# Kernel tuning notes

Hardware: AMD Instinct MI355X
Metric: run time of the kernel (lower is better)

Reference implementation:

```python
import jax, jax.numpy as jnp
import numpy as np
import math

B, H, W, C = 4, 64, 64, 512
G = 32  # GroupNorm groups
EPS = 1e-6


def setup_inputs() -> dict:
    key = jax.random.key(0)
    ks = jax.random.split(key, 6)
    wscale = 1.0 / math.sqrt(C)
    return {
        "x": jax.random.normal(ks[0], (B, H, W, C), jnp.float32),
        "gn_scale": jnp.ones((C,), jnp.float32),
        "gn_bias": jnp.zeros((C,), jnp.float32),
        "wq": jax.random.normal(ks[1], (C, C), jnp.float32) * wscale,
        "bq": jnp.zeros((C,), jnp.float32),
        "wk": jax.random.normal(ks[2], (C, C), jnp.float32) * wscale,
        "bk": jnp.zeros((C,), jnp.float32),
        "wv": jax.random.normal(ks[3], (C, C), jnp.float32) * wscale,
        "bv": jnp.zeros((C,), jnp.float32),
        "wo": jax.random.normal(ks[4], (C, C), jnp.float32) * wscale,
        "bo": jnp.zeros((C,), jnp.float32),
    }


def _group_norm(x, scale, bias):
    # flax nnx.GroupNorm: stats over (H, W, channels-within-group)
    b, h, w, c = x.shape
    xg = x.reshape(b, h, w, G, c // G)
    mean = jnp.mean(xg, axis=(1, 2, 4), keepdims=True)
    var = jnp.mean(jnp.square(xg - mean), axis=(1, 2, 4), keepdims=True)
    xg = (xg - mean) * jax.lax.rsqrt(var + EPS)
    return xg.reshape(b, h, w, c) * scale + bias


def reference(x, gn_scale, gn_bias, wq, bq, wk, bk, wv, bv, wo, bo):
    b, h, w, c = x.shape
    n = h * w
    h_ = _group_norm(x, gn_scale, gn_bias)
    hf = h_.reshape(b, n, c)  # 1x1 conv == per-token matmul
    q = hf @ wq + bq
    k = hf @ wk + bk
    v = hf @ wv + bv
    scale = 1.0 / math.sqrt(c)
    attn = jax.nn.softmax(jnp.einsum('bqc,bkc->bqk', q, k) * scale, axis=-1)
    o = jnp.einsum('bqk,bkc->bqc', attn, v)
    o = o @ wo + bo
    return x + o.reshape(b, h, w, c)
```

## Files before the change

kernel.cpp:

```cpp
#include <hip/hip_runtime.h>
#include <hip/hip_bf16.h>
#include <math.h>


typedef __bf16 bf16;
typedef float f32x4 __attribute__((ext_vector_type(4)));
typedef __bf16 bf16x8 __attribute__((ext_vector_type(8)));
typedef __bf16 bf16x4 __attribute__((ext_vector_type(4)));
typedef long long i64;

#define AS1 __attribute__((address_space(1)))
#define AS3 __attribute__((address_space(3)))

#define NB   4
#define NTOK 4096
#define CCH  512
#define NGRP 32

__device__ __forceinline__ void gload_lds16(const void* g, void* l) {
  __builtin_amdgcn_global_load_lds((AS1 void*)(g), (AS3 void*)(l), 16, 0, 0);
}

__device__ __forceinline__ unsigned char to_e4m3(float f) {
#if __has_builtin(__builtin_amdgcn_cvt_pk_fp8_f32)
  return (unsigned char)(__builtin_amdgcn_cvt_pk_fp8_f32(f, 0.f, 0, false) & 0xff);
#else
  const unsigned u = __float_as_uint(f);
  const unsigned s = (u >> 24) & 0x80;
  const float a = fabsf(f);
  if (a >= 448.f) return (unsigned char)(s | 0x7E);
  if (a < 0.015625f) {
    const int m = (int)rintf(a * 512.f);
    return (unsigned char)(s | m);
  }
  int e = (int)((u >> 23) & 0xff) - 127;
  const float q = exp2f((float)(e - 3));
  int r = (int)rintf(a / q);
  if (r == 16) { e += 1; r = 8; }
  return (unsigned char)(s | ((e + 7) << 3) | (r - 8));
#endif
}

__global__ __launch_bounds__(256) void gn_partial(const float4* __restrict__ x4,
                                                  float* __restrict__ partials) {
  const int chunk = blockIdx.x, b = blockIdx.y;
  const int tid = threadIdx.x;
  const size_t base = ((size_t)b * NTOK + (size_t)chunk * 64) * 128;
  float s = 0.f, ss = 0.f;
  #pragma unroll 4
  for (int it = 0; it < 32; ++it) {
    const float4 v = x4[base + it * 256 + tid];
    s  += v.x + v.y + v.z + v.w;
    ss += v.x * v.x + v.y * v.y + v.z * v.z + v.w * v.w;
  }
  __shared__ float ls[256], lss[256];
  ls[tid] = s; lss[tid] = ss;
  __syncthreads();
  if (tid < 32) {
    float ps = 0.f, pss = 0.f;
    #pragma unroll
    for (int j = 0; j < 4; ++j) {
      ps  += ls[tid * 4 + j] + ls[128 + tid * 4 + j];
      pss += lss[tid * 4 + j] + lss[128 + tid * 4 + j];
    }
    const size_t o = (((size_t)b * 64 + chunk) * 32 + tid) * 2;
    partials[o] = ps; partials[o + 1] = pss;
  }
}

__global__ __launch_bounds__(128) void gn_reduce(const float* __restrict__ partials,
                                                 float* __restrict__ stats) {
  const int tid = threadIdx.x;
  const int b = tid >> 5, g = tid & 31;
  float s = 0.f, ss = 0.f;
  for (int c = 0; c < 64; ++c) {
    const size_t o = (((size_t)b * 64 + c) * 32 + g) * 2;
    s += partials[o]; ss += partials[o + 1];
  }
  const float inv = 1.f / (NTOK * 16.f);
  const float mean = s * inv;
  const float var = ss * inv - mean * mean;
  stats[tid * 2] = mean;
  stats[tid * 2 + 1] = rsqrtf(var + 1e-6f);
}

__global__ __launch_bounds__(256) void gn_apply(const float4* __restrict__ x4,
                                                const float* __restrict__ stats,
                                                const float* __restrict__ gsc,
                                                const float* __restrict__ gbi,
                                                bf16* __restrict__ hf) {
  const int i = blockIdx.x * 256 + threadIdx.x;
  const float4 v = x4[i];
  const size_t e = (size_t)i * 4;
  const int c = (int)(e & (CCH - 1));
  const int b = (int)(e >> 21);
  const int g = c >> 4;
  const float mean = stats[(b * NGRP + g) * 2];
  const float rstd = stats[(b * NGRP + g) * 2 + 1];
  bf16x4 o;
  o[0] = (bf16)((v.x - mean) * rstd * gsc[c + 0] + gbi[c + 0]);
  o[1] = (bf16)((v.y - mean) * rstd * gsc[c + 1] + gbi[c + 1]);
  o[2] = (bf16)((v.z - mean) * rstd * gsc[c + 2] + gbi[c + 2]);
  o[3] = (bf16)((v.w - mean) * rstd * gsc[c + 3] + gbi[c + 3]);
  *reinterpret_cast<bf16x4*>(&hf[e]) = o;
}

__global__ __launch_bounds__(256) void wcast_t(const float* __restrict__ wq,
                                               const float* __restrict__ wk,
                                               const float* __restrict__ bq,
                                               const float* __restrict__ bk,
                                               bf16* __restrict__ dst,
                                               float* __restrict__ bcat) {
  const int w = blockIdx.y;
  const float* src = (w == 0) ? wq : wk;
  bf16* out = dst + (size_t)w * CCH * CCH;
  const int t = blockIdx.x;
  const int tr = t >> 3, tc = t & 7;
  if (t == 0) {
    const float* bsrc = (w == 0) ? bq : bk;
    for (int i = threadIdx.x; i < CCH; i += 256) bcat[w * CCH + i] = bsrc[i];
  }
  __shared__ float tile[64][65];
  for (int i = threadIdx.x; i < 4096; i += 256) {
    const int r = i >> 6, c = i & 63;
    tile[r][c] = src[(size_t)(tr * 64 + r) * CCH + tc * 64 + c];
  }
  __syncthreads();
  for (int i = threadIdx.x; i < 4096; i += 256) {
    const int r = i >> 6, c = i & 63;
    out[(size_t)(tc * 64 + r) * CCH + tr * 64 + c] = (bf16)tile[c][r];
  }
}

__global__ __launch_bounds__(256) void prep_w(const float* __restrict__ wv,
                                              const float* __restrict__ wo,
                                              const float* __restrict__ bv,
                                              const float* __restrict__ bo,
                                              bf16* __restrict__ wpT,
                                              float* __restrict__ bpv) {
  const int ta = blockIdx.x >> 3, tb = blockIdx.x & 7;
  __shared__ float woS[64][65];
  __shared__ float wvS[64][65];
  const int t = threadIdx.x;
  if (blockIdx.x == 0) {
    for (int j = t; j < CCH; j += 256) {
      float a2 = bo[j];
      for (int k2 = 0; k2 < CCH; ++k2) a2 += bv[k2] * wo[(size_t)k2 * CCH + j];
      bpv[j] = a2;
    }
  }
  const int aa0 = (t & 15) * 4, bb0 = (t >> 4) * 4;
  float acc[4][4] = {};
  for (int kt = 0; kt < CCH; kt += 64) {
    for (int i = t; i < 4096; i += 256) {
      const int r = i >> 6, c = i & 63;
      woS[r][c] = wo[(size_t)(kt + r) * CCH + ta * 64 + c];
      wvS[r][c] = wv[(size_t)(tb * 64 + r) * CCH + kt + c];
    }
    __syncthreads();
    #pragma unroll 8
    for (int kk = 0; kk < 64; ++kk) {
      float wo4[4], wv4[4];
      #pragma unroll
      for (int i2 = 0; i2 < 4; ++i2) { wo4[i2] = woS[kk][aa0 + i2]; wv4[i2] = wvS[bb0 + i2][kk]; }
      #pragma unroll
      for (int a2 = 0; a2 < 4; ++a2)
        #pragma unroll
        for (int b2 = 0; b2 < 4; ++b2)
          acc[a2][b2] += wo4[a2] * wv4[b2];
    }
    __syncthreads();
  }
  #pragma unroll
  for (int a2 = 0; a2 < 4; ++a2)
    #pragma unroll
    for (int b2 = 0; b2 < 4; ++b2)
      wpT[(size_t)(ta * 64 + aa0 + a2) * CCH + tb * 64 + bb0 + b2] = (bf16)acc[a2][b2];
}

__global__ __launch_bounds__(256) void rowsum_inv(const float* __restrict__ partials,
                                                  float* __restrict__ rinv) {
  const int row = blockIdx.x * 256 + threadIdx.x;
  const float* p = partials + (size_t)row * 32;
  float s = 0.f;
  #pragma unroll
  for (int j = 0; j < 32; ++j) s += p[j];
  rinv[row] = 1.f / s;
}

template <int EPI>
__global__ __launch_bounds__(512, 2) void gemm256(
    const bf16* __restrict__ A, int lda,
    const bf16* __restrict__ Bt, int ldb,
    unsigned char* __restrict__ C, int ldc,
    const float* __restrict__ bias,
    int M, int N, int K) {
  constexpr int BK = 64;
  constexpr int BNt = 128;
  constexpr int WN = 32;
  constexpr int NREP = 2;

  __shared__ bf16 Al[2][256 * BK];
  __shared__ bf16 Bl[2][BNt * BK];

  const int tid = threadIdx.x;
  const int lane = tid & 63;
  const int wave = tid >> 6;
  const int wm = wave >> 2, wn = wave & 3;
  const int fr = lane & 15, fq = lane >> 4;
  const int nbn = N / BNt;
  int bm, bn;
  if constexpr (EPI == 4) {
    const int nwg = gridDim.x;
    const int bx = (blockIdx.x & 7) * (nwg >> 3) + (blockIdx.x >> 3);
    bm = bx / nbn; bn = bx % nbn;
  } else {
    const int r = blockIdx.x & 7, q = blockIdx.x >> 3;
    const int pg = q / nbn;
    bm = r + 8 * pg;
    bn = q - pg * nbn;
  }

  const int srow = tid >> 3;
  const int scol = (((tid & 7) ^ (srow & 7)) * 8);
  const bf16* Ab = A + (size_t)(bm * 256 + srow) * lda + scol;
  const bf16* Bb = Bt + (size_t)(bn * BNt + srow) * ldb + scol;

  const int xk = fr & 7;
  const int c0 = ((0 + fq) ^ xk) * 8;
  const int c1 = ((4 + fq) ^ xk) * 8;
  const int aroff = (wm * 128 + fr) * BK;
  const int broff = (wn * WN + fr) * BK;

  f32x4 acc[8][NREP];
  #pragma unroll
  for (int m2 = 0; m2 < 8; ++m2)
    #pragma unroll
    for (int n2 = 0; n2 < NREP; ++n2)
      acc[m2][n2] = f32x4{0.f, 0.f, 0.f, 0.f};
  bf16x8 af[4][2];
  bf16x8 bfr[NREP][2];

#define STAGE_A(buf, h, kt)                                                     \
  { gload_lds16(Ab + (size_t)((h) * 128) * lda + (kt),                          \
                &Al[buf][(h) * 8192 + wave * 512]);                             \
    gload_lds16(Ab + (size_t)((h) * 128 + 64) * lda + (kt),                     \
                &Al[buf][(h) * 8192 + 4096 + wave * 512]); }
#define STAGE_B(buf, h, kt)                                                     \
  gload_lds16(Bb + (size_t)((h) * 64) * ldb + (kt),                             \
              &Bl[buf][(h) * 4096 + wave * 512]);
#define LOADA(buf, mh)                                                          \
  { _Pragma("unroll") for (int mi = 0; mi < 4; ++mi) {                          \
      af[mi][0] = *(const bf16x8*)&Al[buf][aroff + ((mh) * 64 + mi * 16) * BK + c0]; \
      af[mi][1] = *(const bf16x8*)&Al[buf][aroff + ((mh) * 64 + mi * 16) * BK + c1]; } }
#define LOADB(buf)                                                              \
  { _Pragma("unroll") for (int ni = 0; ni < NREP; ++ni) {                       \
      bfr[ni][0] = *(const bf16x8*)&Bl[buf][broff + (ni * 16) * BK + c0];       \
      bfr[ni][1] = *(const bf16x8*)&Bl[buf][broff + (ni * 16) * BK + c1]; } }
#define MMA(mh)                                                                 \
  { __builtin_amdgcn_s_setprio(1);                                              \
    _Pragma("unroll") for (int ks = 0; ks < 2; ++ks)                            \
      _Pragma("unroll") for (int mi = 0; mi < 4; ++mi)                          \
        _Pragma("unroll") for (int ni = 0; ni < NREP; ++ni)                     \
          acc[(mh) * 4 + mi][ni] = __builtin_amdgcn_mfma_f32_16x16x32_bf16(     \
              af[mi][ks], bfr[ni][ks], acc[(mh) * 4 + mi][ni], 0, 0, 0);        \
    __builtin_amdgcn_s_setprio(0); }
#define BARX() __builtin_amdgcn_s_barrier()
#define PIN() __builtin_amdgcn_sched_barrier(0)
#define LGKM0() { asm volatile("s_waitcnt lgkmcnt(0)" ::: "memory"); PIN(); }
#define VMW(n) asm volatile("s_waitcnt vmcnt(" #n ")" ::: "memory")

  STAGE_A(0, 0, 0); STAGE_A(0, 1, 0);
  STAGE_B(0, 0, 0); STAGE_B(0, 1, 0);
  STAGE_A(1, 0, BK); STAGE_B(1, 0, BK);
  VMW(3);
  BARX();

  const int niter = K >> 7;
  for (int j = 0; j < niter; ++j) {
    const int kt1 = j * 128 + 64;
    const int kt2 = kt1 + 64, kt3 = kt1 + 128;
    const bool last = (j == niter - 1);
    LOADA(0, 0); LOADB(0); STAGE_A(1, 1, kt1); STAGE_B(1, 1, kt1);
    PIN(); BARX(); LGKM0(); MMA(0); BARX();
    LOADA(0, 1); if (!last) { STAGE_A(0, 0, kt2); STAGE_B(0, 0, kt2); }
    PIN(); BARX(); LGKM0(); MMA(1);
    if (last) { VMW(0); } else VMW(3);
    BARX();
    LOADA(1, 0); LOADB(1); if (!last) { STAGE_A(0, 1, kt2); STAGE_B(0, 1, kt2); }
    PIN(); BARX(); LGKM0(); MMA(0); BARX();
    LOADA(1, 1); if (!last) { STAGE_A(1, 0, kt3); STAGE_B(1, 0, kt3); }
    PIN(); BARX(); LGKM0(); MMA(1);
    if (!last) VMW(3);
    BARX();
  }

  const int crow0 = bm * 256 + wm * 128 + fq * 4;
  const int ccol0 = bn * BNt + wn * WN + fr;
  #pragma unroll
  for (int mh = 0; mh < 2; ++mh)
    #pragma unroll
    for (int mi = 0; mi < 4; ++mi)
      #pragma unroll
      for (int nr = 0; nr < NREP; ++nr)
        #pragma unroll
        for (int jj = 0; jj < 4; ++jj) {
          const int row = crow0 + mh * 64 + mi * 16 + jj;
          const int col = ccol0 + nr * 16;
          const float val = acc[mh * 4 + mi][nr][jj];
          const size_t idx = (size_t)row * ldc + col;
          if constexpr (EPI == 0) {
            C[idx] = to_e4m3(val + bias[col]);
          } else {
            C[idx] = to_e4m3(val);
          }
        }
#undef STAGE_A
#undef STAGE_B
#undef LOADA
#undef LOADB
#undef MMA
#undef BARX
#undef PIN
#undef LGKM0
#undef VMW
}

__global__ __launch_bounds__(512, 4) void scores_fp8(
    const unsigned char* __restrict__ qk,
    unsigned char* __restrict__ S8,
    float* __restrict__ partials,
    float sscale) {
  __shared__ unsigned char Ql[2][16384];
  __shared__ unsigned char Kl[2][8192];
  const int bb = blockIdx.y;
  const unsigned char* Aq = qk + (size_t)bb * NTOK * 1024;
  const int tid = threadIdx.x, lane = tid & 63, wave = tid >> 6;
  const int wm = wave >> 2, wn = wave & 3;
  const int fr = lane & 15, fq = lane >> 4;
  const int r_ = blockIdx.x & 7, q_ = blockIdx.x >> 3;
  const int pg = q_ >> 5;
  const int bm = r_ + 8 * pg, bn = q_ & 31;

  const int sr = tid >> 2;
  const int aswz = ((tid & 3) ^ ((tid >> 3) & 3)) * 16;
  const unsigned char* Ab = Aq + (size_t)(bm * 256 + sr) * 1024 + aswz;
  const unsigned char* Bb = Aq + (size_t)(bn * 128 + sr) * 1024 + 512 + aswz;

  const int xA = fr & 6;
  const int c0 = (fq ^ xA) * 8;
  const int c1 = ((fq ^ 4) ^ xA) * 8;

  f32x4 acc[8][2];
  #pragma unroll
  for (int m2 = 0; m2 < 8; ++m2)
    #pragma unroll
    for (int n2 = 0; n2 < 2; ++n2)
      acc[m2][n2] = f32x4{0.f, 0.f, 0.f, 0.f};
  i64 af8[4][2], bf8[2][2];

#define SSTAGE_A(buf, kt)                                                       \
  { gload_lds16(Ab + (kt), (char*)&Ql[buf][0] + tid * 16);                      \
    gload_lds16(Ab + (size_t)128 * 1024 + (kt), (char*)&Ql[buf][0] + 8192 + tid * 16); }
#define SSTAGE_B(buf, kt)                                                       \
  gload_lds16(Bb + (kt), (char*)&Kl[buf][0] + tid * 16);
#define SLOADA(buf, mh)                                                         \
  { _Pragma("unroll") for (int mi = 0; mi < 4; ++mi) {                          \
      const int ro = (wm * 128 + (mh) * 64 + mi * 16 + fr) * 64;                \
      af8[mi][0] = *(const i64*)&Ql[buf][ro + c0];                              \
      af8[mi][1] = *(const i64*)&Ql[buf][ro + c1]; } }
#define SLOADB(buf)                                                             \
  { _Pragma("unroll") for (int ni = 0; ni < 2; ++ni) {                          \
      const int ro = (wn * 32 + ni * 16 + fr) * 64;                             \
      bf8[ni][0] = *(const i64*)&Kl[buf][ro + c0];                              \
      bf8[ni][1] = *(const i64*)&Kl[buf][ro + c1]; } }
#define SMMA(mh)                                                                \
  { __builtin_amdgcn_s_setprio(1);                                              \
    _Pragma("unroll") for (int ks = 0; ks < 2; ++ks)                            \
      _Pragma("unroll") for (int mi = 0; mi < 4; ++mi)                          \
        _Pragma("unroll") for (int ni = 0; ni < 2; ++ni)                        \
          acc[(mh) * 4 + mi][ni] = __builtin_amdgcn_mfma_f32_16x16x32_fp8_fp8(  \
              af8[mi][ks], bf8[ni][ks], acc[(mh) * 4 + mi][ni], 0, 0, 0);       \
    __builtin_amdgcn_s_setprio(0); }
#define SBARX() __builtin_amdgcn_s_barrier()
#define SPIN() __builtin_amdgcn_sched_barrier(0)
#define SLGKM0() { asm volatile("s_waitcnt lgkmcnt(0)" ::: "memory"); SPIN(); }
#define SVMW(n) asm volatile("s_waitcnt vmcnt(" #n ")" ::: "memory")

  SSTAGE_B(0, 0); SSTAGE_A(0, 0); SSTAGE_B(1, 64);
  SVMW(1);
  SBARX();

  const int niter = 4;
  for (int j = 0; j < niter; ++j) {
    const int kt0 = j * 128;
    const bool last = (j == niter - 1);
    SLOADA(0, 0); SLOADB(0); SSTAGE_A(1, kt0 + 64);
    SPIN(); SBARX(); SLGKM0(); SMMA(0); SBARX();
    SLOADA(0, 1); if (!last) SSTAGE_B(0, kt0 + 128);
    SPIN(); SBARX(); SLGKM0(); SMMA(1);
    if (last) { SVMW(0); } else { SVMW(1); }
    SBARX();
    SLOADA(1, 0); SLOADB(1); if (!last) SSTAGE_A(0, kt0 + 128);
    SPIN(); SBARX(); SLGKM0(); SMMA(0); SBARX();
    SLOADA(1, 1); if (!last) SSTAGE_B(1, kt0 + 192);
    SPIN(); SBARX(); SLGKM0(); SMMA(1);
    if (last) { SVMW(0); } else { SVMW(1); }
    SBARX();
  }

  unsigned char* Cb = S8 + (size_t)bb * NTOK * NTOK;
  const int crow0 = bm * 256 + wm * 128 + fq * 4;
  const int ccol0 = bn * 128 + wn * 32 + fr;
  float* sums = (float*)&Ql[0][0];
  #pragma unroll
  for (int mh = 0; mh < 2; ++mh)
    #pragma unroll
    for (int mi = 0; mi < 4; ++mi)
      #pragma unroll
      for (int jj = 0; jj < 4; ++jj) {
        const int row = crow0 + mh * 64 + mi * 16 + jj;
        float rs = 0.f;
        #pragma unroll
        for (int ni = 0; ni < 2; ++ni) {
          const float e = __expf(fminf(acc[mh * 4 + mi][ni][jj] * sscale, 6.10f));
          rs += e;
          Cb[(size_t)row * NTOK + ccol0 + ni * 16] = to_e4m3(e);
        }
        rs += __shfl_xor(rs, 1); rs += __shfl_xor(rs, 2);
        rs += __shfl_xor(rs, 4); rs += __shfl_xor(rs, 8);
        if (fr == 0)
          sums[(wm * 128 + mh * 64 + mi * 16 + fq * 4 + jj) * 4 + wn] = rs;
      }
  __syncthreads();
  if (tid < 256) {
    const float s4 = sums[tid * 4] + sums[tid * 4 + 1] +
                     sums[tid * 4 + 2] + sums[tid * 4 + 3];
    partials[((size_t)bb * NTOK + bm * 256 + tid) * 32 + bn] = s4;
  }
#undef SSTAGE_A
#undef SSTAGE_B
#undef SLOADA
#undef SLOADB
#undef SMMA
#undef SBARX
#undef SPIN
#undef SLGKM0
#undef SVMW
}

__global__ __launch_bounds__(512, 2) void pv_fp8(
    const unsigned char* __restrict__ S8,
    const unsigned char* __restrict__ V8,
    float* __restrict__ out, const float* __restrict__ bpv,
    const float* __restrict__ x, const float* __restrict__ rinv, int vofs) {
  __shared__ unsigned char Sl[2][16384];
  __shared__ unsigned char Vl[2][8192];
  const int bb = blockIdx.y;
  const unsigned char* A8 = S8 + (size_t)bb * NTOK * NTOK;
  const int tid = threadIdx.x, lane = tid & 63, wave = tid >> 6;
  const int wm = wave >> 2, wn = wave & 3;
  const int fr = lane & 15, fq = lane >> 4;
  const int r_ = blockIdx.x & 7, q_ = blockIdx.x >> 3;
  const int pg = q_ >> 2;
  const int bm = r_ + 8 * pg, bn = q_ & 3;

  const int sr = tid >> 2;
  const int aswz = ((tid & 3) ^ ((tid >> 3) & 3)) * 16;
  const unsigned char* Ab = A8 + (size_t)(bm * 256 + sr) * NTOK + aswz;
  const unsigned char* Bb = V8 + (size_t)(bn * 128 + sr) * (NB * NTOK)
                            + vofs + bb * NTOK + aswz;

  const int xA = fr & 6;
  const int c0 = (fq ^ xA) * 8;
  const int c1 = ((fq ^ 4) ^ xA) * 8;

  f32x4 acc[8][2];
  #pragma unroll
  for (int m2 = 0; m2 < 8; ++m2)
    #pragma unroll
    for (int n2 = 0; n2 < 2; ++n2)
      acc[m2][n2] = f32x4{0.f, 0.f, 0.f, 0.f};
  i64 af8[4][2], bf8[2][2];

#define PSTAGE_A(buf, kt)                                                       \
  { gload_lds16(Ab + (kt), (char*)&Sl[buf][0] + tid * 16);                      \
    gload_lds16(Ab + (size_t)128 * NTOK + (kt), (char*)&Sl[buf][0] + 8192 + tid * 16); }
#define PSTAGE_B(buf, kt)                                                       \
  gload_lds16(Bb + (kt), (char*)&Vl[buf][0] + tid * 16);
#define PLOADA(buf, mh)                                                         \
  { _Pragma("unroll") for (int mi = 0; mi < 4; ++mi) {                          \
      const int ro = (wm * 128 + (mh) * 64 + mi * 16 + fr) * 64;                \
      af8[mi][0] = *(const i64*)&Sl[buf][ro + c0];                              \
      af8[mi][1] = *(const i64*)&Sl[buf][ro + c1]; } }
#define PLOADB(buf)                                                             \
  { _Pragma("unroll") for (int ni = 0; ni < 2; ++ni) {                          \
      const int ro = (wn * 32 + ni * 16 + fr) * 64;                             \
      bf8[ni][0] = *(const i64*)&Vl[buf][ro + c0];                              \
      bf8[ni][1] = *(const i64*)&Vl[buf][ro + c1]; } }
#define PMMA(mh)                                                                \
  { __builtin_amdgcn_s_setprio(1);                                              \
    _Pragma("unroll") for (int ks = 0; ks < 2; ++ks)                            \
      _Pragma("unroll") for (int mi = 0; mi < 4; ++mi)                          \
        _Pragma("unroll") for (int ni = 0; ni < 2; ++ni)                        \
          acc[(mh) * 4 + mi][ni] = __builtin_amdgcn_mfma_f32_16x16x32_fp8_fp8(  \
              af8[mi][ks], bf8[ni][ks], acc[(mh) * 4 + mi][ni], 0, 0, 0);       \
    __builtin_amdgcn_s_setprio(0); }
#define PBARX() __builtin_amdgcn_s_barrier()
#define PPIN() __builtin_amdgcn_sched_barrier(0)
#define PLGKM0() { asm volatile("s_waitcnt lgkmcnt(0)" ::: "memory"); PPIN(); }
#define PVMW(n) asm volatile("s_waitcnt vmcnt(" #n ")" ::: "memory")

  PSTAGE_B(0, 0); PSTAGE_A(0, 0); PSTAGE_B(1, 64);
  PVMW(1);
  PBARX();

  const int niter = 32;
  for (int j = 0; j < niter; ++j) {
    const int kt0 = j * 128;
    const bool last = (j == niter - 1);
    PLOADA(0, 0); PLOADB(0); PSTAGE_A(1, kt0 + 64);
    PPIN(); PBARX(); PLGKM0(); PMMA(0); PBARX();
    PLOADA(0, 1); if (!last) PSTAGE_B(0, kt0 + 128);
    PPIN(); PBARX(); PLGKM0(); PMMA(1);
    if (last) { PVMW(0); } else { PVMW(1); }
    PBARX();
    PLOADA(1, 0); PLOADB(1); if (!last) PSTAGE_A(0, kt0 + 128);
    PPIN(); PBARX(); PLGKM0(); PMMA(0); PBARX();
    PLOADA(1, 1); if (!last) PSTAGE_B(1, kt0 + 192);
    PPIN(); PBARX(); PLGKM0(); PMMA(1);
    if (last) { PVMW(0); } else { PVMW(1); }
    PBARX();
  }

  const int crow0 = bm * 256 + wm * 128 + fq * 4;
  const int ccol0 = bn * 128 + wn * 32 + fr;
  #pragma unroll
  for (int mh = 0; mh < 2; ++mh)
    #pragma unroll
    for (int mi = 0; mi < 4; ++mi)
      #pragma unroll
      for (int jj = 0; jj < 4; ++jj) {
        const int row = crow0 + mh * 64 + mi * 16 + jj;
        const float ri = rinv[(size_t)bb * NTOK + row];
        #pragma unroll
        for (int ni = 0; ni < 2; ++ni) {
          const int col = ccol0 + ni * 16;
          const size_t idx = ((size_t)bb * NTOK + row) * CCH + col;
          out[idx] = acc[mh * 4 + mi][ni][jj] * ri + bpv[col] + x[idx];
        }
      }
#undef PSTAGE_A
#undef PSTAGE_B
#undef PLOADA
#undef PLOADB
#undef PMMA
#undef PBARX
#undef PPIN
#undef PLGKM0
#undef PVMW
}

extern "C" void kernel_launch(void* const* d_in, const int* in_sizes, int n_in,
                              void* d_out, int out_size, void* d_ws, size_t ws_size,
                              hipStream_t stream) {
  const float* x   = (const float*)d_in[0];
  const float* gsc = (const float*)d_in[1];
  const float* gbi = (const float*)d_in[2];
  const float* wq  = (const float*)d_in[3];
  const float* bq  = (const float*)d_in[4];
  const float* wk  = (const float*)d_in[5];
  const float* bk  = (const float*)d_in[6];
  const float* wv  = (const float*)d_in[7];
  const float* bv  = (const float*)d_in[8];
  const float* wo  = (const float*)d_in[9];
  const float* bo  = (const float*)d_in[10];
  float* out = (float*)d_out;
  char* ws = (char*)d_ws;

  const float sscale = 0.044194173824159216f;
  const bool batched = ws_size >= 96082944ULL;

  if (batched) {
    unsigned char* S8  = (unsigned char*)(ws + 0);
    bf16*  hf    = (bf16*)(ws + 0);
    unsigned char* qk8 = (unsigned char*)(ws + 67108864);
    unsigned char* vt8 = (unsigned char*)(ws + 83886080);
    bf16*  wT    = (bf16*)(ws + 92274688);
    float* bcat  = (float*)(ws + 93847552);
    float* bpv   = (float*)(ws + 93851648);
    float* stats = (float*)(ws + 93853696);
    float* parts = (float*)(ws + 93854720);
    float* spart = (float*)(ws + 93920256);
    float* rinv  = (float*)(ws + 96017408);

    gn_partial<<<dim3(64, NB), 256, 0, stream>>>((const float4*)x, parts);
    gn_reduce<<<1, 128, 0, stream>>>(parts, stats);
    gn_apply<<<8192, 256, 0, stream>>>((const float4*)x, stats, gsc, gbi, hf);
    wcast_t<<<dim3(64, 2), 256, 0, stream>>>(wq, wk, bq, bk, wT, bcat);
    prep_w<<<64, 256, 0, stream>>>(wv, wo, bv, bo, wT + 2 * CCH * CCH, bpv);

    gemm256<0><<<dim3(512, 1), 512, 0, stream>>>(
        hf, 512, wT, 512, qk8, 1024, bcat, 16384, 1024, 512);
    gemm256<4><<<dim3(256, 1), 512, 0, stream>>>(
        wT + 2 * CCH * CCH, 512, hf, 512, vt8, 16384, nullptr, 512, 16384, 512);
    scores_fp8<<<dim3(512, NB), 512, 0, stream>>>(qk8, S8, spart, sscale);
    rowsum_inv<<<64, 256, 0, stream>>>(spart, rinv);
    pv_fp8<<<dim3(64, NB), 512, 0, stream>>>(S8, vt8, out, bpv, x, rinv, 0);
  } else {
    unsigned char* S81 = (unsigned char*)(ws + 0);
    bf16*  hf    = (bf16*)(ws + 0);
    unsigned char* qk8 = (unsigned char*)(ws + 16777216);
    unsigned char* vt8 = (unsigned char*)(ws + 33554432);
    bf16*  wT    = (bf16*)(ws + 41943040);
    float* bcat  = (float*)(ws + 43515904);
    float* bpv   = (float*)(ws + 43520000);
    float* stats = (float*)(ws + 43522048);
    float* parts = (float*)(ws + 43523072);
    float* spart = (float*)(ws + 43588608);
    float* rinv  = (float*)(ws + 44112896);

    gn_partial<<<dim3(64, NB), 256, 0, stream>>>((const float4*)x, parts);
    gn_reduce<<<1, 128, 0, stream>>>(parts, stats);
    gn_apply<<<8192, 256, 0, stream>>>((const float4*)x, stats, gsc, gbi, hf);
    wcast_t<<<dim3(64, 2), 256, 0, stream>>>(wq, wk, bq, bk, wT, bcat);
    prep_w<<<64, 256, 0, stream>>>(wv, wo, bv, bo, wT + 2 * CCH * CCH, bpv);
    gemm256<0><<<dim3(512, 1), 512, 0, stream>>>(
        hf, 512, wT, 512, qk8, 1024, bcat, 16384, 1024, 512);
    gemm256<4><<<dim3(256, 1), 512, 0, stream>>>(
        wT + 2 * CCH * CCH, 512, hf, 512, vt8, 16384, nullptr, 512, 16384, 512);
    for (int b = 0; b < NB; ++b) {
      scores_fp8<<<dim3(512, 1), 512, 0, stream>>>(
          qk8 + (size_t)b * NTOK * 1024, S81, spart, sscale);
      rowsum_inv<<<16, 256, 0, stream>>>(spart, rinv);
      pv_fp8<<<dim3(64, 1), 512, 0, stream>>>(
          S81, vt8, out + (size_t)b * NTOK * CCH, bpv,
          x + (size_t)b * NTOK * CCH, rinv, b * NTOK);
    }
  }
}
```

Measured before the change: 288.8 us.

## Permute fp8 K-layout for 16-byte LDS reads and single-buffer 128-wide K tiles

The projection GEMM and the scores kernel now write fp8 outputs with a column permutation inside each 128-wide group. Along with a new 8-way XOR swizzle, this lets the scores and PV kernels fetch both k-steps' MFMA operands with one 16-byte LDS read instead of two 8-byte reads. The double-buffered, barrier-pinned pipeline with 64-wide K stages is replaced by a simple single-buffered loop over 128-wide K tiles that waits for all loads before computing. pv_fp8 occupancy hint rises from 2 to 4 blocks. This cuts LDS instruction count and complexity, but gives up overlap of global loads with MFMA work, which may hurt the long PV loop.

Result: faster. 270.6 us (-6.3%).

```diff
diff --git a/kernel.cpp b/kernel.cpp
--- a/kernel.cpp
+++ b/kernel.cpp
@@ -8,6 +8,7 @@
 typedef __bf16 bf16x8 __attribute__((ext_vector_type(8)));
 typedef __bf16 bf16x4 __attribute__((ext_vector_type(4)));
 typedef long long i64;
+typedef __attribute__((ext_vector_type(2))) long long i64x2;
 
 #define AS1 __attribute__((address_space(1)))
 #define AS3 __attribute__((address_space(3)))
@@ -39,6 +40,12 @@
   if (r == 16) { e += 1; r = 8; }
   return (unsigned char)(s | ((e + 7) << 3) | (r - 8));
 #endif
+}
+
+__device__ __forceinline__ int kperm(int col) {
+  const int g = (col >> 3) & 15;
+  const int gp = (g & 3) * 4 + (g >> 2);
+  return (col & ~127) | (gp * 8) | (col & 7);
 }
 
 __global__ __launch_bounds__(256) void gn_partial(const float4* __restrict__ x4,
@@ -308,7 +315,7 @@
           const int row = crow0 + mh * 64 + mi * 16 + jj;
           const int col = ccol0 + nr * 16;
           const float val = acc[mh * 4 + mi][nr][jj];
-          const size_t idx = (size_t)row * ldc + col;
+          const size_t idx = (size_t)row * ldc + kperm(col);
           if constexpr (EPI == 0) {
             C[idx] = to_e4m3(val + bias[col]);
           } else {
@@ -331,8 +338,8 @@
     unsigned char* __restrict__ S8,
     float* __restrict__ partials,
     float sscale) {
-  __shared__ unsigned char Ql[2][16384];
-  __shared__ unsigned char Kl[2][8192];
+  __shared__ unsigned char Ql[256 * 128];
+  __shared__ unsigned char Kl[128 * 128];
   const int bb = blockIdx.y;
   const unsigned char* Aq = qk + (size_t)bb * NTOK * 1024;
   const int tid = threadIdx.x, lane = tid & 63, wave = tid >> 6;
@@ -342,14 +349,14 @@
   const int pg = q_ >> 5;
   const int bm = r_ + 8 * pg, bn = q_ & 31;
 
-  const int sr = tid >> 2;
-  const int aswz = ((tid & 3) ^ ((tid >> 3) & 3)) * 16;
-  const unsigned char* Ab = Aq + (size_t)(bm * 256 + sr) * 1024 + aswz;
-  const unsigned char* Bb = Aq + (size_t)(bn * 128 + sr) * 1024 + 512 + aswz;
-
-  const int xA = fr & 6;
-  const int c0 = (fq ^ xA) * 8;
-  const int c1 = ((fq ^ 4) ^ xA) * 8;
+  const int sr = tid >> 3;
+  const int ssl = ((tid & 7) ^ (sr & 7)) * 16;
+  const unsigned char* Ab = Aq + (size_t)(bm * 256 + sr) * 1024 + ssl;
+  const unsigned char* Bb = Aq + (size_t)(bn * 128 + sr) * 1024 + 512 + ssl;
+
+  const int xk = fr & 7;
+  const int sA0 = ((2 * fq + 0) ^ xk) * 16;
+  const int sA1 = ((2 * fq + 1) ^ xk) * 16;
 
   f32x4 acc[8][2];
   #pragma unroll
@@ -357,62 +364,49 @@
     #pragma unroll
     for (int n2 = 0; n2 < 2; ++n2)
       acc[m2][n2] = f32x4{0.f, 0.f, 0.f, 0.f};
-  i64 af8[4][2], bf8[2][2];
-
-#define SSTAGE_A(buf, kt)                                                       \
-  { gload_lds16(Ab + (kt), (char*)&Ql[buf][0] + tid * 16);                      \
-    gload_lds16(Ab + (size_t)128 * 1024 + (kt), (char*)&Ql[buf][0] + 8192 + tid * 16); }
-#define SSTAGE_B(buf, kt)                                                       \
-  gload_lds16(Bb + (kt), (char*)&Kl[buf][0] + tid * 16);
-#define SLOADA(buf, mh)                                                         \
-  { _Pragma("unroll") for (int mi = 0; mi < 4; ++mi) {                          \
-      const int ro = (wm * 128 + (mh) * 64 + mi * 16 + fr) * 64;                \
-      af8[mi][0] = *(const i64*)&Ql[buf][ro + c0];                              \
-      af8[mi][1] = *(const i64*)&Ql[buf][ro + c1]; } }
-#define SLOADB(buf)                                                             \
-  { _Pragma("unroll") for (int ni = 0; ni < 2; ++ni) {                          \
-      const int ro = (wn * 32 + ni * 16 + fr) * 64;                             \
-      bf8[ni][0] = *(const i64*)&Kl[buf][ro + c0];                              \
-      bf8[ni][1] = *(const i64*)&Kl[buf][ro + c1]; } }
-#define SMMA(mh)                                                                \
-  { __builtin_amdgcn_s_setprio(1);                                              \
-    _Pragma("unroll") for (int ks = 0; ks < 2; ++ks)                            \
-      _Pragma("unroll") for (int mi = 0; mi < 4; ++mi)                          \
-        _Pragma("unroll") for (int ni = 0; ni < 2; ++ni)                        \
-          acc[(mh) * 4 + mi][ni] = __builtin_amdgcn_mfma_f32_16x16x32_fp8_fp8(  \
-              af8[mi][ks], bf8[ni][ks], acc[(mh) * 4 + mi][ni], 0, 0, 0);       \
-    __builtin_amdgcn_s_setprio(0); }
-#define SBARX() __builtin_amdgcn_s_barrier()
-#define SPIN() __builtin_amdgcn_sched_barrier(0)
-#define SLGKM0() { asm volatile("s_waitcnt lgkmcnt(0)" ::: "memory"); SPIN(); }
-#define SVMW(n) asm volatile("s_waitcnt vmcnt(" #n ")" ::: "memory")
-
-  SSTAGE_B(0, 0); SSTAGE_A(0, 0); SSTAGE_B(1, 64);
-  SVMW(1);
-  SBARX();
-
-  const int niter = 4;
-  for (int j = 0; j < niter; ++j) {
-    const int kt0 = j * 128;
-    const bool last = (j == niter - 1);
-    SLOADA(0, 0); SLOADB(0); SSTAGE_A(1, kt0 + 64);
-    SPIN(); SBARX(); SLGKM0(); SMMA(0); SBARX();
-    SLOADA(0, 1); if (!last) SSTAGE_B(0, kt0 + 128);
-    SPIN(); SBARX(); SLGKM0(); SMMA(1);
-    if (last) { SVMW(0); } else { SVMW(1); }
-    SBARX();
-    SLOADA(1, 0); SLOADB(1); if (!last) SSTAGE_A(0, kt0 + 128);
-    SPIN(); SBARX(); SLGKM0(); SMMA(0); SBARX();
-    SLOADA(1, 1); if (!last) SSTAGE_B(1, kt0 + 192);
-    SPIN(); SBARX(); SLGKM0(); SMMA(1);
-    if (last) { SVMW(0); } else { SVMW(1); }
-    SBARX();
+
+  for (int it = 0; it < 4; ++it) {
+    const int kt = it * 128;
+    #pragma unroll
+    for (int i = 0; i < 4; ++i)
+      gload_lds16(Ab + (size_t)(i * 64) * 1024 + kt, (char*)Ql + i * 8192 + tid * 16);
+    #pragma unroll
+    for (int i = 0; i < 2; ++i)
+      gload_lds16(Bb + (size_t)(i * 64) * 1024 + kt, (char*)Kl + i * 8192 + tid * 16);
+    asm volatile("s_waitcnt vmcnt(0)" ::: "memory");
+    __syncthreads();
+    #pragma unroll
+    for (int t = 0; t < 2; ++t) {
+      const int sl = (t == 0) ? sA0 : sA1;
+      i64x2 bfv[2];
+      #pragma unroll
+      for (int ni = 0; ni < 2; ++ni)
+        bfv[ni] = *(const i64x2*)&Kl[(wn * 32 + ni * 16 + fr) * 128 + sl];
+      #pragma unroll
+      for (int mh = 0; mh < 2; ++mh) {
+        i64x2 afv[4];
+        #pragma unroll
+        for (int mi = 0; mi < 4; ++mi)
+          afv[mi] = *(const i64x2*)&Ql[(wm * 128 + mh * 64 + mi * 16 + fr) * 128 + sl];
+        __builtin_amdgcn_s_setprio(1);
+        #pragma unroll
+        for (int ks = 0; ks < 2; ++ks)
+          #pragma unroll
+          for (int mi = 0; mi < 4; ++mi)
+            #pragma unroll
+            for (int ni = 0; ni < 2; ++ni)
+              acc[mh * 4 + mi][ni] = __builtin_amdgcn_mfma_f32_16x16x32_fp8_fp8(
+                  afv[mi][ks], bfv[ni][ks], acc[mh * 4 + mi][ni], 0, 0, 0);
+        __builtin_amdgcn_s_setprio(0);
+      }
+    }
+    __syncthreads();
   }
 
   unsigned char* Cb = S8 + (size_t)bb * NTOK * NTOK;
   const int crow0 = bm * 256 + wm * 128 + fq * 4;
   const int ccol0 = bn * 128 + wn * 32 + fr;
-  float* sums = (float*)&Ql[0][0];
+  float* sums = (float*)&Ql[0];
   #pragma unroll
   for (int mh = 0; mh < 2; ++mh)
     #pragma unroll
@@ -425,7 +419,7 @@
         for (int ni = 0; ni < 2; ++ni) {
           const float e = __expf(fminf(acc[mh * 4 + mi][ni][jj] * sscale, 6.10f));
           rs += e;
-          Cb[(size_t)row * NTOK + ccol0 + ni * 16] = to_e4m3(e);
+          Cb[(size_t)row * NTOK + kperm(ccol0 + ni * 16)] = to_e4m3(e);
         }
         rs += __shfl_xor(rs, 1); rs += __shfl_xor(rs, 2);
         rs += __shfl_xor(rs, 4); rs += __shfl_xor(rs, 8);
@@ -438,24 +432,15 @@
                      sums[tid * 4 + 2] + sums[tid * 4 + 3];
     partials[((size_t)bb * NTOK + bm * 256 + tid) * 32 + bn] = s4;
   }
-#undef SSTAGE_A
-#undef SSTAGE_B
-#undef SLOADA
-#undef SLOADB
-#undef SMMA
-#undef SBARX
-#undef SPIN
-#undef SLGKM0
-#undef SVMW
-}
-
-__global__ __launch_bounds__(512, 2) void pv_fp8(
+}
+
+__global__ __launch_bounds__(512, 4) void pv_fp8(
     const unsigned char* __restrict__ S8,
     const unsigned char* __restrict__ V8,
     float* __restrict__ out, const float* __restrict__ bpv,
     const float* __restrict__ x, const float* __restrict__ rinv, int vofs) {
-  __shared__ unsigned char Sl[2][16384];
-  __shared__ unsigned char Vl[2][8192];
+  __shared__ unsigned char Sl[256 * 128];
+  __shared__ unsigned char Vl[128 * 128];
   const int bb = blockIdx.y;
   const unsigned char* A8 = S8 + (size_t)bb * NTOK * NTOK;
   const int tid = threadIdx.x, lane = tid & 63, wave = tid >> 6;
@@ -465,15 +450,15 @@
   const int pg = q_ >> 2;
   const int bm = r_ + 8 * pg, bn = q_ & 3;
 
-  const int sr = tid >> 2;
-  const int aswz = ((tid & 3) ^ ((tid >> 3) & 3)) * 16;
-  const unsigned char* Ab = A8 + (size_t)(bm * 256 + sr) * NTOK + aswz;
+  const int sr = tid >> 3;
+  const int ssl = ((tid & 7) ^ (sr & 7)) * 16;
+  const unsigned char* Ab = A8 + (size_t)(bm * 256 + sr) * NTOK + ssl;
   const unsigned char* Bb = V8 + (size_t)(bn * 128 + sr) * (NB * NTOK)
-                            + vofs + bb * NTOK + aswz;
-
-  const int xA = fr & 6;
-  const int c0 = (fq ^ xA) * 8;
-  const int c1 = ((fq ^ 4) ^ xA) * 8;
+                            + vofs + bb * NTOK + ssl;
+
+  const int xk = fr & 7;
+  const int sA0 = ((2 * fq + 0) ^ xk) * 16;
+  const int sA1 = ((2 * fq + 1) ^ xk) * 16;
 
   f32x4 acc[8][2];
   #pragma unroll
@@ -481,56 +466,43 @@
     #pragma unroll
     for (int n2 = 0; n2 < 2; ++n2)
       acc[m2][n2] = f32x4{0.f, 0.f, 0.f, 0.f};
-  i64 af8[4][2], bf8[2][2];
-
-#define PSTAGE_A(buf, kt)                                                       \
-  { gload_lds16(Ab + (kt), (char*)&Sl[buf][0] + tid * 16);                      \
-    gload_lds16(Ab + (size_t)128 * NTOK + (kt), (char*)&Sl[buf][0] + 8192 + tid * 16); }
-#define PSTAGE_B(buf, kt)                                                       \
-  gload_lds16(Bb + (kt), (char*)&Vl[buf][0] + tid * 16);
-#define PLOADA(buf, mh)                                                         \
-  { _Pragma("unroll") for (int mi = 0; mi < 4; ++mi) {                          \
-      const int ro = (wm * 128 + (mh) * 64 + mi * 16 + fr) * 64;                \
-      af8[mi][0] = *(const i64*)&Sl[buf][ro + c0];                              \
-      af8[mi][1] = *(const i64*)&Sl[buf][ro + c1]; } }
-#define PLOADB(buf)                                                             \
-  { _Pragma("unroll") for (int ni = 0; ni < 2; ++ni) {                          \
-      const int ro = (wn * 32 + ni * 16 + fr) * 64;                             \
-      bf8[ni][0] = *(const i64*)&Vl[buf][ro + c0];                              \
-      bf8[ni][1] = *(const i64*)&Vl[buf][ro + c1]; } }
-#define PMMA(mh)                                                                \
-  { __builtin_amdgcn_s_setprio(1);                                              \
-    _Pragma("unroll") for (int ks = 0; ks < 2; ++ks)                            \
-      _Pragma("unroll") for (int mi = 0; mi < 4; ++mi)                          \
-        _Pragma("unroll") for (int ni = 0; ni < 2; ++ni)                        \
-          acc[(mh) * 4 + mi][ni] = __builtin_amdgcn_mfma_f32_16x16x32_fp8_fp8(  \
-              af8[mi][ks], bf8[ni][ks], acc[(mh) * 4 + mi][ni], 0, 0, 0);       \
-    __builtin_amdgcn_s_setprio(0); }
-#define PBARX() __builtin_amdgcn_s_barrier()
-#define PPIN() __builtin_amdgcn_sched_barrier(0)
-#define PLGKM0() { asm volatile("s_waitcnt lgkmcnt(0)" ::: "memory"); PPIN(); }
-#define PVMW(n) asm volatile("s_waitcnt vmcnt(" #n ")" ::: "memory")
-
-  PSTAGE_B(0, 0); PSTAGE_A(0, 0); PSTAGE_B(1, 64);
-  PVMW(1);
-  PBARX();
-
-  const int niter = 32;
-  for (int j = 0; j < niter; ++j) {
-    const int kt0 = j * 128;
-    const bool last = (j == niter - 1);
-    PLOADA(0, 0); PLOADB(0); PSTAGE_A(1, kt0 + 64);
-    PPIN(); PBARX(); PLGKM0(); PMMA(0); PBARX();
-    PLOADA(0, 1); if (!last) PSTAGE_B(0, kt0 + 128);
-    PPIN(); PBARX(); PLGKM0(); PMMA(1);
-    if (last) { PVMW(0); } else { PVMW(1); }
-    PBARX();
-    PLOADA(1, 0); PLOADB(1); if (!last) PSTAGE_A(0, kt0 + 128);
-    PPIN(); PBARX(); PLGKM0(); PMMA(0); PBARX();
-    PLOADA(1, 1); if (!last) PSTAGE_B(1, kt0 + 192);
-    PPIN(); PBARX(); PLGKM0(); PMMA(1);
-    if (last) { PVMW(0); } else { PVMW(1); }
-    PBARX();
+
+  for (int it = 0; it < 32; ++it) {
+    const int kt = it * 128;
+    #pragma unroll
+    for (int i = 0; i < 4; ++i)
+      gload_lds16(Ab + (size_t)(i * 64) * NTOK + kt, (char*)Sl + i * 8192 + tid * 16);
+    #pragma unroll
+    for (int i = 0; i < 2; ++i)
+      gload_lds16(Bb + (size_t)(i * 64) * (NB * NTOK) + kt, (char*)Vl + i * 8192 + tid * 16);
+    asm volatile("s_waitcnt vmcnt(0)" ::: "memory");
+    __syncthreads();
+    #pragma unroll
+    for (int t = 0; t < 2; ++t) {
+      const int sl = (t == 0) ? sA0 : sA1;
+      i64x2 bfv[2];
+      #pragma unroll
+      for (int ni = 0; ni < 2; ++ni)
+        bfv[ni] = *(const i64x2*)&Vl[(wn * 32 + ni * 16 + fr) * 128 + sl];
+      #pragma unroll
+      for (int mh = 0; mh < 2; ++mh) {
+        i64x2 afv[4];
+        #pragma unroll
+        for (int mi = 0; mi < 4; ++mi)
+          afv[mi] = *(const i64x2*)&Sl[(wm * 128 + mh * 64 + mi * 16 + fr) * 128 + sl];
+        __builtin_amdgcn_s_setprio(1);
+        #pragma unroll
+        for (int ks = 0; ks < 2; ++ks)
+          #pragma unroll
+          for (int mi = 0; mi < 4; ++mi)
+            #pragma unroll
+            for (int ni = 0; ni < 2; ++ni)
+              acc[mh * 4 + mi][ni] = __builtin_amdgcn_mfma_f32_16x16x32_fp8_fp8(
+                  afv[mi][ks], bfv[ni][ks], acc[mh * 4 + mi][ni], 0, 0, 0);
+        __builtin_amdgcn_s_setprio(0);
+      }
+    }
+    __syncthreads();
   }
 
   const int crow0 = bm * 256 + wm * 128 + fq * 4;
@@ -550,15 +522,6 @@
           out[idx] = acc[mh * 4 + mi][ni][jj] * ri + bpv[col] + x[idx];
         }
       }
-#undef PSTAGE_A
-#undef PSTAGE_B
-#undef PLOADA
-#undef PLOADB
-#undef PMMA
-#undef PBARX
-#undef PPIN
-#undef PLGKM0
-#undef PVMW
 }
 
 extern "C" void kernel_launch(void* const* d_in, const int* in_sizes, int n_in,
```
